# Kernel tuning notes

Hardware: AMD Instinct MI355X
Metric: run time of the kernel (lower is better)

Reference implementation:

```python
import jax, jax.numpy as jnp
import numpy as np

D_MODEL = 1024
N_HEADS = 16
HEAD_DIM = D_MODEL // N_HEADS
D_FF = 4 * D_MODEL
LN_EPS = 1e-5


def setup_inputs() -> dict:
    key = jax.random.key(0)
    ks = jax.random.split(key, 12)
    B, T = 16, 512
    s = lambda fan_in: 1.0 / np.sqrt(fan_in)
    inp = {
        'x': jax.random.normal(ks[0], (B, T, D_MODEL), jnp.float32),
        # torch Linear layout: [out_features, in_features]
        'w_qkv': jax.random.normal(ks[1], (3 * D_MODEL, D_MODEL), jnp.float32) * s(D_MODEL),
        'w_proj': jax.random.normal(ks[2], (D_MODEL, D_MODEL), jnp.float32) * s(D_MODEL),
        'w_ff1': jax.random.normal(ks[3], (D_FF, D_MODEL), jnp.float32) * s(D_MODEL),
        'b_ff1': jax.random.normal(ks[4], (D_FF,), jnp.float32) * 0.02,
        'w_ff2': jax.random.normal(ks[5], (D_MODEL, D_FF), jnp.float32) * s(D_FF),
        'b_ff2': jax.random.normal(ks[6], (D_MODEL,), jnp.float32) * 0.02,
        'ln1_g': jnp.ones((D_MODEL,), jnp.float32),
        'ln1_b': jnp.zeros((D_MODEL,), jnp.float32),
        'ln2_g': jnp.ones((D_MODEL,), jnp.float32),
        'ln2_b': jnp.zeros((D_MODEL,), jnp.float32),
    }
    return inp


def _layernorm(x, g, b):
    mu = jnp.mean(x, axis=-1, keepdims=True)
    var = jnp.var(x, axis=-1, keepdims=True)
    return (x - mu) * jax.lax.rsqrt(var + LN_EPS) * g + b


def _block(x, w_qkv, w_proj, w_ff1, b_ff1, w_ff2, b_ff2, ln1_g, ln1_b, ln2_g, ln2_b):
    B, T, _ = x.shape
    a = _layernorm(x, ln1_g, ln1_b)
    qkv = a @ w_qkv.T  # [B,T,3D]
    q, k, v = jnp.split(qkv, 3, axis=-1)
    # [B,H,T,hd]
    rs = lambda t: t.reshape(B, T, N_HEADS, HEAD_DIM).transpose(0, 2, 1, 3)
    q, k, v = rs(q), rs(k), rs(v)
    scale = HEAD_DIM ** -0.5
    att = jnp.einsum('bhqd,bhkd->bhqk', q, k) * scale
    causal = jnp.tril(jnp.ones((T, T), bool))
    att = jnp.where(causal, att, jnp.float32(-10000.0))
    att = jax.nn.softmax(att, axis=-1)
    out = jnp.einsum('bhqk,bhkd->bhqd', att, v)
    out = out.transpose(0, 2, 1, 3).reshape(B, T, D_MODEL)
    x = x + out @ w_proj.T
    f = _layernorm(x, ln2_g, ln2_b)
    f = jax.nn.gelu(f @ w_ff1.T + b_ff1, approximate=False) @ w_ff2.T + b_ff2
    return x + f


def reference(x, w_qkv, w_proj, w_ff1, b_ff1, w_ff2, b_ff2, ln1_g, ln1_b, ln2_g, ln2_b):
    return _block(x, w_qkv, w_proj, w_ff1, b_ff1, w_ff2, b_ff2, ln1_g, ln1_b, ln2_g, ln2_b)
```

## Files before the change

### kernel.cpp

```cpp
#include <hip/hip_runtime.h>
#include <stdint.h>

typedef __bf16 bf16x8_t __attribute__((ext_vector_type(8)));
typedef float f32x4_t __attribute__((ext_vector_type(4)));

#define DEV __device__ __forceinline__

DEV unsigned short f2bf(float f) {
  union { float f; uint32_t u; } v; v.f = f;
  uint32_t r = v.u + 0x7FFFu + ((v.u >> 16) & 1u);
  return (unsigned short)(r >> 16);
}

DEV void gl_lds16(const void* g, void* l) {
  __builtin_amdgcn_global_load_lds(
      (const __attribute__((address_space(1))) void*)g,
      (__attribute__((address_space(3))) void*)l, 16, 0, 0);
}

DEV void barx() {
  asm volatile("" ::: "memory");
  __builtin_amdgcn_s_barrier();
  asm volatile("" ::: "memory");
}

DEV float gelu_f(float x) {
  const float y = x * 0.7071067811865475f;
  const float ay = fabsf(y);
  const float t = __builtin_amdgcn_rcpf(1.0f + 0.3275911f * ay);
  float p = fmaf(t, 1.061405429f, -1.453152027f);
  p = fmaf(t, p, 1.421413741f);
  p = fmaf(t, p, -0.284496736f);
  p = fmaf(t, p, 0.254829592f);
  p *= t;
  const float e = __expf(-ay * ay);
  float erfv = 1.0f - p * e;
  erfv = copysignf(erfv, y);
  return 0.5f * x * (1.0f + erfv);
}

__global__ __launch_bounds__(256) void cvt_all(const float* __restrict__ w0, unsigned short* __restrict__ o0,
                                               const float* __restrict__ w1, unsigned short* __restrict__ o1,
                                               const float* __restrict__ w2, unsigned short* __restrict__ o2,
                                               const float* __restrict__ w3, unsigned short* __restrict__ o3) {
  int i = blockIdx.x * 256 + threadIdx.x;
  const float* in; unsigned short* outp;
  if (i < 786432) { in = w0; outp = o0; }
  else if (i < 1048576) { in = w1; outp = o1; i -= 786432; }
  else if (i < 2097152) { in = w2; outp = o2; i -= 1048576; }
  else { in = w3; outp = o3; i -= 2097152; }
  float4 v = ((const float4*)in)[i];
  ushort4 o;
  o.x = f2bf(v.x); o.y = f2bf(v.y); o.z = f2bf(v.z); o.w = f2bf(v.w);
  ((ushort4*)outp)[i] = o;
}

__global__ __launch_bounds__(256) void ln_kernel(const float* __restrict__ x,
                                                 const float* __restrict__ g,
                                                 const float* __restrict__ b,
                                                 unsigned short* __restrict__ outp) {
  const int row = blockIdx.x * 4 + (threadIdx.x >> 6);
  const int lane = threadIdx.x & 63;
  const float4* xr = (const float4*)(x + (size_t)row * 1024);
  float4 v[4];
  float s = 0.f, s2 = 0.f;
#pragma unroll
  for (int j = 0; j < 4; ++j) {
    v[j] = xr[j * 64 + lane];
    s += v[j].x + v[j].y + v[j].z + v[j].w;
    s2 += v[j].x * v[j].x + v[j].y * v[j].y + v[j].z * v[j].z + v[j].w * v[j].w;
  }
#pragma unroll
  for (int off = 1; off < 64; off <<= 1) {
    s += __shfl_xor(s, off, 64);
    s2 += __shfl_xor(s2, off, 64);
  }
  const float mu = s * (1.0f / 1024.0f);
  const float var = s2 * (1.0f / 1024.0f) - mu * mu;
  const float rstd = rsqrtf(var + 1e-5f);
  ushort4* orow = (ushort4*)(outp + (size_t)row * 1024);
  const float4* gp = (const float4*)g;
  const float4* bp = (const float4*)b;
#pragma unroll
  for (int j = 0; j < 4; ++j) {
    float4 gv = gp[j * 64 + lane], bv = bp[j * 64 + lane];
    ushort4 o;
    o.x = f2bf((v[j].x - mu) * rstd * gv.x + bv.x);
    o.y = f2bf((v[j].y - mu) * rstd * gv.y + bv.y);
    o.z = f2bf((v[j].z - mu) * rstd * gv.z + bv.z);
    o.w = f2bf((v[j].w - mu) * rstd * gv.w + bv.w);
    orow[j * 64 + lane] = o;
  }
}


#define RD_A(MH, PC)                                                        \
  _Pragma("unroll") for (int mi = 0; mi < 4; ++mi)                          \
      a[mi] = *(const bf16x8_t*)(pA + (wm + (MH)*64 + mi * 16 + l16) * 64 + (PC));

#define RD_B(DST, PC)                                                       \
  _Pragma("unroll") for (int ni = 0; ni < 4; ++ni)                          \
      DST[ni] = *(const bf16x8_t*)(pB + (wn + ni * 16 + l16) * 64 + (PC));

#define MFMA16(MH, BB)                                                      \
  __builtin_amdgcn_s_setprio(1);                                            \
  _Pragma("unroll") for (int mi = 0; mi < 4; ++mi)                          \
  _Pragma("unroll") for (int ni = 0; ni < 4; ++ni)                          \
      acc[(MH)*4 + mi][ni] = __builtin_amdgcn_mfma_f32_16x16x32_bf16(       \
          a[mi], BB[ni], acc[(MH)*4 + mi][ni], 0, 0, 0);                    \
  __builtin_amdgcn_s_setprio(0);

template <int MODE>
__global__ __launch_bounds__(512) void gemm8(const unsigned short* __restrict__ A,
                                             const unsigned short* __restrict__ B,
                                             float* __restrict__ Cf,
                                             unsigned short* __restrict__ Cb,
                                             const float* __restrict__ bias,
                                             const float* __restrict__ res,
                                             unsigned short* __restrict__ Vt,
                                             int M, int N, int K) {
  __shared__ unsigned short sA[2][256 * 64];
  __shared__ unsigned short sB[2][256 * 64];
  const int tid = threadIdx.x;
  const int w = tid >> 6, lane = tid & 63;
  const int kg = lane >> 4, l16 = lane & 15;
  const int wm = (w & 1) * 128, wn = (w >> 1) * 64;

  const int nwg = gridDim.x;
  const int bid = blockIdx.x;
  const int cid = (bid & 7) * (nwg >> 3) + (bid >> 3);
  const int rowBase = (cid & 31) * 256;
  const int colBase = (cid >> 5) * 256;

  const int srow = tid >> 3, sch = tid & 7;
  const unsigned short* aBase = A + (size_t)(rowBase + srow) * K + ((sch ^ (srow & 7)) * 8);
  const unsigned short* bBase = B + (size_t)(colBase + srow) * K + ((sch ^ (srow & 7)) * 8);
  const int sdo = tid * 8;

  f32x4_t acc[8][4];
#pragma unroll
  for (int mi = 0; mi < 8; ++mi)
#pragma unroll
    for (int ni = 0; ni < 4; ++ni) acc[mi][ni] = (f32x4_t)0.0f;

  const int nt = K >> 6;
  const int pc0 = ((kg ^ (l16 & 7)) & 7) * 8;
  const int pc1 = (((4 + kg) ^ (l16 & 7)) & 7) * 8;

#pragma unroll
  for (int R = 0; R < 4; ++R)
    gl_lds16(aBase + (size_t)(R * 64) * K, &sA[0][R * 4096 + sdo]);
#pragma unroll
  for (int Cq = 0; Cq < 4; ++Cq)
    gl_lds16(bBase + (size_t)(Cq * 64) * K, &sB[0][Cq * 4096 + sdo]);
  {
    const size_t k1 = (nt > 1) ? 64 : 0;
    gl_lds16(aBase + k1, &sA[1][sdo]);
    gl_lds16(aBase + (size_t)128 * K + k1, &sA[1][8192 + sdo]);
  }
  asm volatile("s_waitcnt vmcnt(2)" ::: "memory");
  barx();

  for (int kt = 0; kt < nt; ++kt) {
    const int cur = kt & 1;
    const unsigned short* pA = &sA[cur][0];
    const unsigned short* pB = &sB[cur][0];
    unsigned short* nAd = &sA[cur ^ 1][0];
    unsigned short* nBd = &sB[cur ^ 1][0];
    unsigned short* pAd = &sA[cur][0];
    const size_t kA1 = (size_t)((kt + 1 < nt) ? (kt + 1) : (nt - 1)) * 64;
    const size_t kA2 = (size_t)((kt + 2 < nt) ? (kt + 2) : 0) * 64;

    bf16x8_t a[4], b0[4], b1[4];

    RD_A(0, pc0)
    RD_B(b0, pc0)
    gl_lds16(aBase + (size_t)64 * K + kA1, nAd + 4096 + sdo);
    gl_lds16(aBase + (size_t)192 * K + kA1, nAd + 12288 + sdo);
    barx();
    MFMA16(0, b0)
    barx();

    RD_A(0, pc1)
    RD_B(b1, pc1)
    gl_lds16(bBase + kA1, nBd + sdo);
    gl_lds16(bBase + (size_t)64 * K + kA1, nBd + 4096 + sdo);
    barx();
    MFMA16(0, b1)
    barx();

    RD_A(1, pc0)
    gl_lds16(bBase + (size_t)128 * K + kA1, nBd + 8192 + sdo);
    gl_lds16(bBase + (size_t)192 * K + kA1, nBd + 12288 + sdo);
    barx();
    MFMA16(1, b0)
    barx();

    RD_A(1, pc1)
    gl_lds16(aBase + kA2, pAd + sdo);
    gl_lds16(aBase + (size_t)128 * K + kA2, pAd + 8192 + sdo);
    barx();
    MFMA16(1, b1)
    asm volatile("s_waitcnt vmcnt(2)" ::: "memory");
    barx();
  }

#pragma unroll
  for (int mi = 0; mi < 8; ++mi) {
#pragma unroll
    for (int ni = 0; ni < 4; ++ni) {
      const int col = colBase + wn + ni * 16 + l16;
      if (MODE == 0 && colBase >= 2048) {
        const int c2 = col - 2048;
        const int hh = c2 >> 6, dd = c2 & 63;
        const int rw = rowBase + wm + mi * 16 + kg * 4;
        ushort4 pk;
        pk.x = f2bf(acc[mi][ni][0]);
        pk.y = f2bf(acc[mi][ni][1]);
        pk.z = f2bf(acc[mi][ni][2]);
        pk.w = f2bf(acc[mi][ni][3]);
        *(ushort4*)(Vt + (((size_t)(rw >> 9) * 16 + hh) * 64 + dd) * 512 + (rw & 511)) = pk;
        continue;
      }
      float bv = 0.f;
      if (MODE == 2 || MODE == 3) bv = bias[col];
#pragma unroll
      for (int r = 0; r < 4; ++r) {
        const int row = rowBase + wm + mi * 16 + kg * 4 + r;
        const size_t idx = (size_t)row * N + col;
        float v = acc[mi][ni][r];
        if (MODE == 0) {
          Cb[idx] = f2bf(v);
        } else if (MODE == 1) {
          Cf[idx] = v + res[idx];
        } else if (MODE == 2) {
          Cb[idx] = f2bf(gelu_f(v + bv));
        } else {
          Cf[idx] = v + bv + res[idx];
        }
      }
    }
  }
  asm volatile("s_waitcnt vmcnt(0)" ::: "memory");
}

__global__ __launch_bounds__(256) void attn_kernel(const unsigned short* __restrict__ qkv,
                                                   const unsigned short* __restrict__ Vt,
                                                   unsigned short* __restrict__ outp) {
  constexpr int D3 = 3072;
  __shared__ unsigned short sQ[128 * 64];
  __shared__ unsigned short sK[64 * 64];
  __shared__ unsigned short sVt[64 * 64];
  __shared__ unsigned short sP[128 * 72];
  const int tid = threadIdx.x;
  const int w = tid >> 6, lane = tid & 63;
  const int kg = lane >> 4, l16 = lane & 15;
  const int qi = (int)gridDim.x - 1 - (int)blockIdx.x;
  const int h = blockIdx.y, bb = blockIdx.z;
  const int t0 = qi * 128;
  const size_t base = (size_t)bb * 512 * D3 + h * 64;

  const int sr = tid >> 3;
  const int sc = ((tid & 7) ^ (sr & 7)) * 8;

  {
    const unsigned short* g = qkv + base + (size_t)(t0 + sr) * D3 + sc;
    unsigned short* l = sQ + tid * 8;
#pragma unroll
    for (int i = 0; i < 4; ++i) gl_lds16(g + (size_t)32 * i * D3, l + 2048 * i);
  }

  const unsigned short* gVbase = Vt + ((size_t)(bb * 16 + h) * 64 + sr) * 512 + sc;

  bf16x8_t ones;
#pragma unroll
  for (int j = 0; j < 8; ++j) ones[j] = (__bf16)1.0f;

  const int wm = w * 32;
  f32x4_t o[2][4];
  f32x4_t lsum[2];
#pragma unroll
  for (int mi = 0; mi < 2; ++mi) {
    lsum[mi] = (f32x4_t)0.0f;
#pragma unroll
    for (int di = 0; di < 4; ++di) o[mi][di] = (f32x4_t)0.0f;
  }

  const int nkt = (qi + 1) * 2;
  for (int kt = 0; kt < nkt; ++kt) {
    const int k0 = kt * 64;
    __syncthreads();
    {
      const unsigned short* g = qkv + base + 1024 + (size_t)(k0 + sr) * D3 + sc;
      unsigned short* l = sK + tid * 8;
      gl_lds16(g, l);
      gl_lds16(g + (size_t)32 * D3, l + 2048);
    }
    {
      const unsigned short* g = gVbase + k0;
      unsigned short* l = sVt + tid * 8;
      gl_lds16(g, l);
      gl_lds16(g + (size_t)32 * 512, l + 2048);
    }
    __syncthreads();

    const bool active = (k0 <= t0 + wm + 31);
    if (active) {
      f32x4_t s[2][4];
#pragma unroll
      for (int mi = 0; mi < 2; ++mi)
#pragma unroll
        for (int ni = 0; ni < 4; ++ni) s[mi][ni] = (f32x4_t)0.0f;
#pragma unroll
      for (int kd = 0; kd < 2; ++kd) {
        bf16x8_t aq[2], bk[4];
#pragma unroll
        for (int mi = 0; mi < 2; ++mi) {
          const int rr = wm + mi * 16 + l16;
          aq[mi] = *(const bf16x8_t*)(sQ + rr * 64 + (((kd * 4 + kg) ^ (l16 & 7)) * 8));
        }
#pragma unroll
        for (int ni = 0; ni < 4; ++ni) {
          const int rr = ni * 16 + l16;
          bk[ni] = *(const bf16x8_t*)(sK + rr * 64 + (((kd * 4 + kg) ^ (l16 & 7)) * 8));
        }
#pragma unroll
        for (int mi = 0; mi < 2; ++mi)
#pragma unroll
          for (int ni = 0; ni < 4; ++ni)
            s[mi][ni] = __builtin_amdgcn_mfma_f32_16x16x32_bf16(aq[mi], bk[ni], s[mi][ni], 0, 0, 0);
      }
#pragma unroll
      for (int mi = 0; mi < 2; ++mi) {
#pragma unroll
        for (int r = 0; r < 4; ++r) {
          const int q = t0 + wm + mi * 16 + kg * 4 + r;
          const int prow = wm + mi * 16 + kg * 4 + r;
#pragma unroll
          for (int ni = 0; ni < 4; ++ni) {
            const int kk = k0 + ni * 16 + l16;
            const float p = (kk <= q) ? __expf(s[mi][ni][r] * 0.125f) : 0.0f;
            sP[prow * 72 + ni * 16 + l16] = f2bf(p);
          }
        }
      }
#pragma unroll
      for (int kd = 0; kd < 2; ++kd) {
        bf16x8_t ap[2], bv[4];
#pragma unroll
        for (int mi = 0; mi < 2; ++mi)
          ap[mi] = *(const bf16x8_t*)(sP + (wm + mi * 16 + l16) * 72 + kd * 32 + kg * 8);
#pragma unroll
        for (int di = 0; di < 4; ++di) {
          const int dd = di * 16 + l16;
          bv[di] = *(const bf16x8_t*)(sVt + dd * 64 + (((kd * 4 + kg) ^ (l16 & 7)) * 8));
        }
#pragma unroll
        for (int mi = 0; mi < 2; ++mi) {
#pragma unroll
          for (int di = 0; di < 4; ++di)
            o[mi][di] = __builtin_amdgcn_mfma_f32_16x16x32_bf16(ap[mi], bv[di], o[mi][di], 0, 0, 0);
          lsum[mi] = __builtin_amdgcn_mfma_f32_16x16x32_bf16(ap[mi], ones, lsum[mi], 0, 0, 0);
        }
      }
    }
  }

#pragma unroll
  for (int mi = 0; mi < 2; ++mi) {
#pragma unroll
    for (int r = 0; r < 4; ++r) {
      const float inv = 1.0f / lsum[mi][r];
      const int row = t0 + wm + mi * 16 + kg * 4 + r;
      const size_t ob = ((size_t)bb * 512 + row) * 1024 + h * 64;
#pragma unroll
      for (int di = 0; di < 4; ++di)
        outp[ob + di * 16 + l16] = f2bf(o[mi][di][r] * inv);
    }
  }
}

extern "C" void kernel_launch(void* const* d_in, const int* in_sizes, int n_in,
                              void* d_out, int out_size, void* d_ws, size_t ws_size,
                              hipStream_t stream) {
  const float* x      = (const float*)d_in[0];
  const float* w_qkv  = (const float*)d_in[1];
  const float* w_proj = (const float*)d_in[2];
  const float* w_ff1  = (const float*)d_in[3];
  const float* b_ff1  = (const float*)d_in[4];
  const float* w_ff2  = (const float*)d_in[5];
  const float* b_ff2  = (const float*)d_in[6];
  const float* ln1_g  = (const float*)d_in[7];
  const float* ln1_b  = (const float*)d_in[8];
  const float* ln2_g  = (const float*)d_in[9];
  const float* ln2_b  = (const float*)d_in[10];
  float* out = (float*)d_out;
  char* ws = (char*)d_ws;

  unsigned short* wqkv_b  = (unsigned short*)(ws + 0);
  unsigned short* wproj_b = (unsigned short*)(ws + 6291456);
  unsigned short* wff1_b  = (unsigned short*)(ws + 8388608);
  unsigned short* wff2_b  = (unsigned short*)(ws + 16777216);
  unsigned short* a_b     = (unsigned short*)(ws + 25165824);
  float*          x2_f    = (float*)(ws + 41943040);
  unsigned short* vt_b    = (unsigned short*)(ws + 41943040);
  unsigned short* qkv_b   = (unsigned short*)(ws + 75497472);
  unsigned short* attn_b  = (unsigned short*)(ws + 125829120);
  unsigned short* h_b     = qkv_b;

  cvt_all<<<12288, 256, 0, stream>>>(w_qkv, wqkv_b, w_proj, wproj_b, w_ff1, wff1_b, w_ff2, wff2_b);

  ln_kernel<<<2048, 256, 0, stream>>>(x, ln1_g, ln1_b, a_b);
  gemm8<0><<<384, 512, 0, stream>>>(a_b, wqkv_b, nullptr, qkv_b, nullptr, nullptr, vt_b, 8192, 3072, 1024);
  attn_kernel<<<dim3(4, 16, 16), 256, 0, stream>>>(qkv_b, vt_b, attn_b);
  gemm8<1><<<128, 512, 0, stream>>>(attn_b, wproj_b, x2_f, nullptr, nullptr, x, nullptr, 8192, 1024, 1024);
  ln_kernel<<<2048, 256, 0, stream>>>(x2_f, ln2_g, ln2_b, a_b);
  gemm8<2><<<512, 512, 0, stream>>>(a_b, wff1_b, nullptr, h_b, b_ff1, nullptr, nullptr, 8192, 4096, 1024);
  gemm8<3><<<128, 512, 0, stream>>>(h_b, wff2_b, out, nullptr, b_ff2, x2_f, nullptr, 8192, 1024, 4096);
}
```

Baseline: 530.6 us.

## Split-K the FF2 GEMM and restructure GEMM main loop with register prefetch

Rewrites the GEMM main loop as a two-tile unrolled pipeline. The A and B fragments for the next step are read from LDS ahead of the MFMAs, DMA issue is spread across phases, and waits use explicit vmcnt counts. The FF2 GEMM (K=4096, only 128 workgroups) is split into two K halves across 256 workgroups. The second half writes fp32 partials to scratch buffers, and a new elementwise kernel adds them into the output. This is meant to raise CU occupancy on the under-filled FF2 GEMM and hide LDS latency, at the cost of extra partial-sum traffic and one more launch.

```diff
diff --git a/kernel.cpp b/kernel.cpp
--- a/kernel.cpp
+++ b/kernel.cpp
@@ -23,6 +23,8 @@
   __builtin_amdgcn_s_barrier();
   asm volatile("" ::: "memory");
 }
+
+#define VMC(N) asm volatile("s_waitcnt vmcnt(" #N ")" ::: "memory")
 
 DEV float gelu_f(float x) {
   const float y = x * 0.7071067811865475f;
@@ -94,21 +96,52 @@
 }
 
 
-#define RD_A(MH, PC)                                                        \
-  _Pragma("unroll") for (int mi = 0; mi < 4; ++mi)                          \
-      a[mi] = *(const bf16x8_t*)(pA + (wm + (MH)*64 + mi * 16 + l16) * 64 + (PC));
-
-#define RD_B(DST, PC)                                                       \
-  _Pragma("unroll") for (int ni = 0; ni < 4; ++ni)                          \
-      DST[ni] = *(const bf16x8_t*)(pB + (wn + ni * 16 + l16) * 64 + (PC));
-
-#define MFMA16(MH, BB)                                                      \
-  __builtin_amdgcn_s_setprio(1);                                            \
-  _Pragma("unroll") for (int mi = 0; mi < 4; ++mi)                          \
-  _Pragma("unroll") for (int ni = 0; ni < 4; ++ni)                          \
-      acc[(MH)*4 + mi][ni] = __builtin_amdgcn_mfma_f32_16x16x32_bf16(       \
-          a[mi], BB[ni], acc[(MH)*4 + mi][ni], 0, 0, 0);                    \
+#define RD_AF(DST, BUF, MH, PC)                                               \
+  _Pragma("unroll") for (int mi = 0; mi < 4; ++mi)                            \
+      DST[mi] = *(const bf16x8_t*)((BUF) + (wm + (MH)*64 + mi * 16 + l16) * 64 + (PC));
+
+#define RD_BF(DST, BUF, PC)                                                   \
+  _Pragma("unroll") for (int ni = 0; ni < 4; ++ni)                            \
+      DST[ni] = *(const bf16x8_t*)((BUF) + (wn + ni * 16 + l16) * 64 + (PC));
+
+#define MFMA16(MH, AA, BB)                                                    \
+  __builtin_amdgcn_s_setprio(1);                                              \
+  _Pragma("unroll") for (int mi = 0; mi < 4; ++mi)                            \
+  _Pragma("unroll") for (int ni = 0; ni < 4; ++ni)                            \
+      acc[(MH)*4 + mi][ni] = __builtin_amdgcn_mfma_f32_16x16x32_bf16(         \
+          AA[mi], BB[ni], acc[(MH)*4 + mi][ni], 0, 0, 0);                     \
   __builtin_amdgcn_s_setprio(0);
+
+#define DMA_A(BUF, Q, KT) gl_lds16(aBase + (size_t)((Q)*64) * lda + (size_t)(KT)*64, &sA[BUF][(Q)*4096 + sdo])
+#define DMA_B(BUF, Q, KT) gl_lds16(bBase + (size_t)((Q)*64) * lda + (size_t)(KT)*64, &sB[BUF][(Q)*4096 + sdo])
+
+#define TILE(T, CB, B0c, B1c, B0n)                                            \
+  {                                                                           \
+    const int t1 = ((T) + 1 < nt) ? (T) + 1 : nt - 1;                         \
+    const int t2 = ((T) + 2 < nt) ? (T) + 2 : nt - 1;                         \
+    const unsigned short* pA = &sA[CB][0];                                    \
+    const unsigned short* pB = &sB[CB][0];                                    \
+                                                                     \
+    barx(); VMC(8);                                                           \
+    RD_AF(aO, pA, 0, pc1) RD_BF(B1c, pB, pc1)                                 \
+    MFMA16(0, aE, B0c)                                                        \
+    DMA_A(CB ^ 1, 1, t1); DMA_A(CB ^ 1, 3, t1);                               \
+                                                                     \
+    barx(); VMC(8);                                                           \
+    RD_AF(aE, pA, 1, pc0)                                                     \
+    MFMA16(0, aO, B1c)                                                        \
+    DMA_B(CB, 0, t2); DMA_B(CB, 1, t2);                                       \
+                                                                     \
+    barx();                                                                   \
+    RD_AF(aO, pA, 1, pc1)                                                     \
+    MFMA16(1, aE, B0c)                                                        \
+    DMA_A(CB, 0, t2); DMA_A(CB, 2, t2);                                       \
+                                                                     \
+    barx(); VMC(6);                                                           \
+    RD_AF(aE, &sA[CB ^ 1][0], 0, pc0) RD_BF(B0n, &sB[CB ^ 1][0], pc0)         \
+    MFMA16(1, aO, B1c)                                                        \
+    DMA_B(CB, 2, t2); DMA_B(CB, 3, t2);                                       \
+  }
 
 template <int MODE>
 __global__ __launch_bounds__(512) void gemm8(const unsigned short* __restrict__ A,
@@ -118,7 +151,7 @@
                                              const float* __restrict__ bias,
                                              const float* __restrict__ res,
                                              unsigned short* __restrict__ Vt,
-                                             int M, int N, int K) {
+                                             int M, int N, int K, int lda) {
   __shared__ unsigned short sA[2][256 * 64];
   __shared__ unsigned short sB[2][256 * 64];
   const int tid = threadIdx.x;
@@ -129,12 +162,15 @@
   const int nwg = gridDim.x;
   const int bid = blockIdx.x;
   const int cid = (bid & 7) * (nwg >> 3) + (bid >> 3);
-  const int rowBase = (cid & 31) * 256;
-  const int colBase = (cid >> 5) * 256;
+  int ks = 0, cc = cid;
+  if (MODE == 4) { ks = cid >> 7; cc = cid & 127; }
+  const int rowBase = (cc & 31) * 256;
+  const int colBase = (cc >> 5) * 256;
+  const int koff = ks * K;
 
   const int srow = tid >> 3, sch = tid & 7;
-  const unsigned short* aBase = A + (size_t)(rowBase + srow) * K + ((sch ^ (srow & 7)) * 8);
-  const unsigned short* bBase = B + (size_t)(colBase + srow) * K + ((sch ^ (srow & 7)) * 8);
+  const unsigned short* aBase = A + (size_t)(rowBase + srow) * lda + koff + ((sch ^ (srow & 7)) * 8);
+  const unsigned short* bBase = B + (size_t)(colBase + srow) * lda + koff + ((sch ^ (srow & 7)) * 8);
   const int sdo = tid * 8;
 
   f32x4_t acc[8][4];
@@ -147,62 +183,26 @@
   const int pc0 = ((kg ^ (l16 & 7)) & 7) * 8;
   const int pc1 = (((4 + kg) ^ (l16 & 7)) & 7) * 8;
 
-#pragma unroll
-  for (int R = 0; R < 4; ++R)
-    gl_lds16(aBase + (size_t)(R * 64) * K, &sA[0][R * 4096 + sdo]);
-#pragma unroll
-  for (int Cq = 0; Cq < 4; ++Cq)
-    gl_lds16(bBase + (size_t)(Cq * 64) * K, &sB[0][Cq * 4096 + sdo]);
+  bf16x8_t aE[4], aO[4], B0a[4], B1a[4], B0b[4], B1b[4];
+
   {
-    const size_t k1 = (nt > 1) ? 64 : 0;
-    gl_lds16(aBase + k1, &sA[1][sdo]);
-    gl_lds16(aBase + (size_t)128 * K + k1, &sA[1][8192 + sdo]);
-  }
-  asm volatile("s_waitcnt vmcnt(2)" ::: "memory");
+    const int t1p = 1 < nt ? 1 : 0;
+#pragma unroll
+    for (int q = 0; q < 4; ++q) DMA_A(0, q, 0);
+#pragma unroll
+    for (int q = 0; q < 4; ++q) DMA_B(0, q, 0);
+    DMA_A(1, 0, t1p); DMA_A(1, 2, t1p);
+#pragma unroll
+    for (int q = 0; q < 4; ++q) DMA_B(1, q, t1p);
+  }
+  VMC(6);
   barx();
-
-  for (int kt = 0; kt < nt; ++kt) {
-    const int cur = kt & 1;
-    const unsigned short* pA = &sA[cur][0];
-    const unsigned short* pB = &sB[cur][0];
-    unsigned short* nAd = &sA[cur ^ 1][0];
-    unsigned short* nBd = &sB[cur ^ 1][0];
-    unsigned short* pAd = &sA[cur][0];
-    const size_t kA1 = (size_t)((kt + 1 < nt) ? (kt + 1) : (nt - 1)) * 64;
-    const size_t kA2 = (size_t)((kt + 2 < nt) ? (kt + 2) : 0) * 64;
-
-    bf16x8_t a[4], b0[4], b1[4];
-
-    RD_A(0, pc0)
-    RD_B(b0, pc0)
-    gl_lds16(aBase + (size_t)64 * K + kA1, nAd + 4096 + sdo);
-    gl_lds16(aBase + (size_t)192 * K + kA1, nAd + 12288 + sdo);
-    barx();
-    MFMA16(0, b0)
-    barx();
-
-    RD_A(0, pc1)
-    RD_B(b1, pc1)
-    gl_lds16(bBase + kA1, nBd + sdo);
-    gl_lds16(bBase + (size_t)64 * K + kA1, nBd + 4096 + sdo);
-    barx();
-    MFMA16(0, b1)
-    barx();
-
-    RD_A(1, pc0)
-    gl_lds16(bBase + (size_t)128 * K + kA1, nBd + 8192 + sdo);
-    gl_lds16(bBase + (size_t)192 * K + kA1, nBd + 12288 + sdo);
-    barx();
-    MFMA16(1, b0)
-    barx();
-
-    RD_A(1, pc1)
-    gl_lds16(aBase + kA2, pAd + sdo);
-    gl_lds16(aBase + (size_t)128 * K + kA2, pAd + 8192 + sdo);
-    barx();
-    MFMA16(1, b1)
-    asm volatile("s_waitcnt vmcnt(2)" ::: "memory");
-    barx();
+  RD_AF(aE, &sA[0][0], 0, pc0)
+  RD_BF(B0a, &sB[0][0], pc0)
+
+  for (int t = 0; t < nt; t += 2) {
+    TILE(t, 0, B0a, B1a, B0b)
+    TILE(t + 1, 1, B0b, B1b, B0a)
   }
 
 #pragma unroll
@@ -223,7 +223,7 @@
         continue;
       }
       float bv = 0.f;
-      if (MODE == 2 || MODE == 3) bv = bias[col];
+      if (MODE == 2 || MODE == 3 || (MODE == 4 && ks == 0)) bv = bias[col];
 #pragma unroll
       for (int r = 0; r < 4; ++r) {
         const int row = rowBase + wm + mi * 16 + kg * 4 + r;
@@ -235,13 +235,30 @@
           Cf[idx] = v + res[idx];
         } else if (MODE == 2) {
           Cb[idx] = f2bf(gelu_f(v + bv));
+        } else if (MODE == 3) {
+          Cf[idx] = v + bv + res[idx];
         } else {
-          Cf[idx] = v + bv + res[idx];
+          if (ks == 0) {
+            Cf[idx] = v + bv + res[idx];
+          } else {
+            float* P = (rowBase < 4096) ? (float*)Cb : (float*)Vt;
+            P[(size_t)((row & 4095)) * N + col] = v;
+          }
         }
       }
     }
   }
   asm volatile("s_waitcnt vmcnt(0)" ::: "memory");
+}
+
+__global__ __launch_bounds__(256) void ff2_fin(float* __restrict__ outp,
+                                               const float* __restrict__ p1a,
+                                               const float* __restrict__ p1b) {
+  const int i = blockIdx.x * 256 + threadIdx.x;
+  float4 v = ((float4*)outp)[i];
+  const float4 p = (i < 1048576) ? ((const float4*)p1a)[i] : ((const float4*)p1b)[i - 1048576];
+  v.x += p.x; v.y += p.y; v.z += p.z; v.w += p.w;
+  ((float4*)outp)[i] = v;
 }
 
 __global__ __launch_bounds__(256) void attn_kernel(const unsigned short* __restrict__ qkv,
@@ -407,14 +424,17 @@
   unsigned short* qkv_b   = (unsigned short*)(ws + 75497472);
   unsigned short* attn_b  = (unsigned short*)(ws + 125829120);
   unsigned short* h_b     = qkv_b;
+  float* p1a = (float*)a_b;
+  float* p1b = (float*)attn_b;
 
   cvt_all<<<12288, 256, 0, stream>>>(w_qkv, wqkv_b, w_proj, wproj_b, w_ff1, wff1_b, w_ff2, wff2_b);
 
   ln_kernel<<<2048, 256, 0, stream>>>(x, ln1_g, ln1_b, a_b);
-  gemm8<0><<<384, 512, 0, stream>>>(a_b, wqkv_b, nullptr, qkv_b, nullptr, nullptr, vt_b, 8192, 3072, 1024);
+  gemm8<0><<<384, 512, 0, stream>>>(a_b, wqkv_b, nullptr, qkv_b, nullptr, nullptr, vt_b, 8192, 3072, 1024, 1024);
   attn_kernel<<<dim3(4, 16, 16), 256, 0, stream>>>(qkv_b, vt_b, attn_b);
-  gemm8<1><<<128, 512, 0, stream>>>(attn_b, wproj_b, x2_f, nullptr, nullptr, x, nullptr, 8192, 1024, 1024);
+  gemm8<1><<<128, 512, 0, stream>>>(attn_b, wproj_b, x2_f, nullptr, nullptr, x, nullptr, 8192, 1024, 1024, 1024);
   ln_kernel<<<2048, 256, 0, stream>>>(x2_f, ln2_g, ln2_b, a_b);
-  gemm8<2><<<512, 512, 0, stream>>>(a_b, wff1_b, nullptr, h_b, b_ff1, nullptr, nullptr, 8192, 4096, 1024);
-  gemm8<3><<<128, 512, 0, stream>>>(h_b, wff2_b, out, nullptr, b_ff2, x2_f, nullptr, 8192, 1024, 4096);
-}
+  gemm8<2><<<512, 512, 0, stream>>>(a_b, wff1_b, nullptr, h_b, b_ff1, nullptr, nullptr, 8192, 4096, 1024, 1024);
+  gemm8<4><<<256, 512, 0, stream>>>(h_b, wff2_b, out, (unsigned short*)p1a, b_ff2, x2_f, (unsigned short*)p1b, 8192, 1024, 2048, 4096);
+  ff2_fin<<<8192, 256, 0, stream>>>(out, p1a, p1b);
+}
```

New measurement: 484.9 us. 1.09x faster.
